# Optimization experiments

Hardware: AMD Instinct MI355X
Metric: run time of the kernel (lower is better)

## Reference

```python
import jax, jax.numpy as jnp
import numpy as np

D_MODEL = 1024
N_HEADS = 16
D_HEAD = D_MODEL // N_HEADS
LN_EPS = 1e-5


def setup_inputs() -> dict:
    key = jax.random.key(0)
    ks = jax.random.split(key, 6)
    B, T = 2, 2048
    s_in = 1.0 / np.sqrt(D_MODEL)
    return {
        "x": jax.random.normal(ks[0], (B, T, D_MODEL), dtype=jnp.float32),
        "ln_g": jnp.ones((D_MODEL,), jnp.float32),
        "ln_b": jnp.zeros((D_MODEL,), jnp.float32),
        "qkv_w": jax.random.normal(ks[1], (D_MODEL, 3 * D_MODEL), jnp.float32) * s_in,
        "qkv_b": jnp.zeros((3 * D_MODEL,), jnp.float32),
        "out_w": jax.random.normal(ks[2], (D_MODEL, D_MODEL), jnp.float32) * s_in,
        "out_b": jnp.zeros((D_MODEL,), jnp.float32),
    }


def _layernorm(x, g, b):
    mu = jnp.mean(x, axis=-1, keepdims=True)
    var = jnp.var(x, axis=-1, keepdims=True)
    return (x - mu) * jax.lax.rsqrt(var + LN_EPS) * g + b


def reference(x, ln_g, ln_b, qkv_w, qkv_b, out_w, out_b):
    B, T, D = x.shape
    h = _layernorm(x, ln_g, ln_b)
    qkv = h @ qkv_w + qkv_b  # [B,T,3D]
    q, k, v = jnp.split(qkv, 3, axis=-1)
    # [B,H,T,dh]
    q = q.reshape(B, T, N_HEADS, D_HEAD).transpose(0, 2, 1, 3)
    k = k.reshape(B, T, N_HEADS, D_HEAD).transpose(0, 2, 1, 3)
    v = v.reshape(B, T, N_HEADS, D_HEAD).transpose(0, 2, 1, 3)
    scores = jnp.einsum("bhqd,bhkd->bhqk", q, k) / jnp.sqrt(jnp.float32(D_HEAD))
    causal = jnp.tril(jnp.ones((T, T), bool))
    scores = jnp.where(causal, scores, -jnp.inf)
    attn = jax.nn.softmax(scores, axis=-1)  # [B,H,T,T]
    out = jnp.einsum("bhqk,bhkd->bhqd", attn, v)
    out = out.transpose(0, 2, 1, 3).reshape(B, T, D)
    x_out = x + out @ out_w + out_b
    return (x_out, attn)
```

## Files before the change

### kernel.cpp

```cpp
#include <hip/hip_runtime.h>
#include <math.h>

#define B_SZ 2
#define T_SEQ 2048
#define DM 1024
#define NH 16
#define DH 64
#define ROWS (B_SZ * T_SEQ)
#define LN_EPS 1e-5f

typedef __attribute__((ext_vector_type(8))) short short8;
typedef __attribute__((ext_vector_type(4))) float floatx4;

__device__ __forceinline__ short f2bf(float f) {
    union { float f; unsigned u; } v; v.f = f;
    unsigned r = v.u + 0x7fffu + ((v.u >> 16) & 1u);
    return (short)(r >> 16);
}
__device__ __forceinline__ short8 ld8(const short* p) {
    short4 a = *(const short4*)p;
    short4 b = *(const short4*)(p + 4);
    return short8{a.x, a.y, a.z, a.w, b.x, b.y, b.z, b.w};
}
__device__ __forceinline__ void gl2lds16(const void* g, void* l) {
    __builtin_amdgcn_global_load_lds(
        (const __attribute__((address_space(1))) unsigned int*)g,
        (__attribute__((address_space(3))) unsigned int*)l, 16, 0, 0);
}

__global__ __launch_bounds__(256) void ln_kernel(const float* __restrict__ x,
                                                 const float* __restrict__ g,
                                                 const float* __restrict__ bta,
                                                 short* __restrict__ h) {
    int row = blockIdx.x;
    const float* xr = x + (size_t)row * DM;
    int tid = threadIdx.x;
    float4 v = ((const float4*)xr)[tid];
    float s = v.x + v.y + v.z + v.w;
    float ss = v.x * v.x + v.y * v.y + v.z * v.z + v.w * v.w;
    for (int off = 1; off < 64; off <<= 1) {
        s += __shfl_xor(s, off);
        ss += __shfl_xor(ss, off);
    }
    __shared__ float sbuf[4], ssbuf[4];
    int wave = tid >> 6, lane = tid & 63;
    if (lane == 0) { sbuf[wave] = s; ssbuf[wave] = ss; }
    __syncthreads();
    s = sbuf[0] + sbuf[1] + sbuf[2] + sbuf[3];
    ss = ssbuf[0] + ssbuf[1] + ssbuf[2] + ssbuf[3];
    float mu = s * (1.0f / DM);
    float var = ss * (1.0f / DM) - mu * mu;
    float rs = rsqrtf(var + LN_EPS);
    float4 gg = ((const float4*)g)[tid];
    float4 bb = ((const float4*)bta)[tid];
    short4 o;
    o.x = f2bf((v.x - mu) * rs * gg.x + bb.x);
    o.y = f2bf((v.y - mu) * rs * gg.y + bb.y);
    o.z = f2bf((v.z - mu) * rs * gg.z + bb.z);
    o.w = f2bf((v.w - mu) * rs * gg.w + bb.w);
    *(short4*)&h[(size_t)row * DM + tid * 4] = o;
}

__global__ __launch_bounds__(256) void wt_kernel(const float* __restrict__ W,
                                                 short* __restrict__ Wt, int K, int N) {
    __shared__ float t[32][33];
    int tx = threadIdx.x & 31, ty = threadIdx.x >> 5;
    int k0 = blockIdx.y * 32, n0 = blockIdx.x * 32;
    for (int p = 0; p < 4; ++p)
        t[ty + 8 * p][tx] = W[(size_t)(k0 + ty + 8 * p) * N + n0 + tx];
    __syncthreads();
    for (int p = 0; p < 4; ++p)
        Wt[(size_t)(n0 + ty + 8 * p) * K + k0 + tx] = f2bf(t[tx][ty + 8 * p]);
}

template <bool RESID, bool BF16_OUT>
__global__ __launch_bounds__(256) void mfma_gemm(const short* __restrict__ A,
                                                 const short* __restrict__ Bt,
                                                 const float* __restrict__ bias,
                                                 const float* __restrict__ resid,
                                                 void* __restrict__ Cout,
                                                 int M, int N, int K) {
    __shared__ short As[128 * 32];
    __shared__ short Bs[128 * 32];
    int tid = threadIdx.x;
    int wave = tid >> 6, lane = tid & 63;
    int l15 = lane & 15, quad = lane >> 4;
    int wm = wave & 1, wn = wave >> 1;
    int row0 = blockIdx.y * 128, col0 = blockIdx.x * 128;

    floatx4 acc[4][4] = {};
    for (int k0 = 0; k0 < K; k0 += 32) {
        __syncthreads();
        for (int i = 0; i < 2; ++i) {
            int c = (wave * 2 + i) * 64 + lane;
            int row = c >> 2, kc = c & 3;
            gl2lds16(A + (size_t)(row0 + row) * K + k0 + kc * 8, &As[(wave * 2 + i) * 512]);
            gl2lds16(Bt + (size_t)(col0 + row) * K + k0 + kc * 8, &Bs[(wave * 2 + i) * 512]);
        }
        __syncthreads();
        short8 af[4], bfr[4];
        for (int m = 0; m < 4; ++m)
            af[m] = *(const short8*)&As[(wm * 64 + m * 16 + l15) * 32 + quad * 8];
        for (int n = 0; n < 4; ++n)
            bfr[n] = *(const short8*)&Bs[(wn * 64 + n * 16 + l15) * 32 + quad * 8];
        for (int m = 0; m < 4; ++m)
            for (int n = 0; n < 4; ++n)
                acc[m][n] = __builtin_amdgcn_mfma_f32_16x16x32_bf16(af[m], bfr[n], acc[m][n], 0, 0, 0);
    }
    float bias_v[4];
    for (int n = 0; n < 4; ++n) bias_v[n] = bias[col0 + wn * 64 + n * 16 + l15];
    for (int m = 0; m < 4; ++m)
        for (int r = 0; r < 4; ++r) {
            int rg = row0 + wm * 64 + m * 16 + quad * 4 + r;
            for (int n = 0; n < 4; ++n) {
                int cg = col0 + wn * 64 + n * 16 + l15;
                float v = acc[m][n][r] + bias_v[n];
                if (BF16_OUT) {
                    ((short*)Cout)[(size_t)rg * N + cg] = f2bf(v);
                } else {
                    if (RESID) v += resid[(size_t)rg * N + cg];
                    ((float*)Cout)[(size_t)rg * N + cg] = v;
                }
            }
        }
}

__global__ __launch_bounds__(256) void vt_kernel(const short* __restrict__ qkv,
                                                 short* __restrict__ Vt) {
    int bh = blockIdx.y;
    int b = bh >> 4, hh = bh & 15;
    int t0 = blockIdx.x * 64;
    __shared__ short tile[64 * 72];
    int tc = threadIdx.x & 7, tr = threadIdx.x >> 3;
    const short* src = qkv + (size_t)(b * T_SEQ + t0) * (3 * DM) + 2 * DM + hh * DH;
    for (int p = 0; p < 2; ++p) {
        int r = tr + p * 32;
        *(short8*)&tile[r * 72 + tc * 8] = *(const short8*)(src + (size_t)r * (3 * DM) + tc * 8);
    }
    __syncthreads();
    short* dst = Vt + (size_t)bh * DH * T_SEQ + t0;
    for (int p = 0; p < 2; ++p) {
        int d = tr + p * 32;
        short tmp[8];
#pragma unroll
        for (int j = 0; j < 8; ++j) tmp[j] = tile[(tc * 8 + j) * 72 + d];
        *(short8*)(dst + (size_t)d * T_SEQ + tc * 8) =
            short8{tmp[0], tmp[1], tmp[2], tmp[3], tmp[4], tmp[5], tmp[6], tmp[7]};
    }
}

__global__ __launch_bounds__(256) void attn_kernel(const short* __restrict__ qkv,
                                                   const short* __restrict__ Vt,
                                                   float* __restrict__ attn,
                                                   short* __restrict__ ao) {
    int blk = blockIdx.x;
    int qt = (T_SEQ / 64 - 1) - (blk & 31);
    int bh = blk >> 5;
    int b = bh >> 4, hh = bh & 15;
    int q0 = qt * 64;
    int tid = threadIdx.x;
    int wave = tid >> 6, lane = tid & 63;
    int l15 = lane & 15, quad = lane >> 4;

    __shared__ short Ks[64 * 64];
    __shared__ short Vs[64 * 64];
    __shared__ short Ps[4 * 16 * 72];

    const float scale = 0.125f;
    const short* Qg = qkv + (size_t)(b * T_SEQ + q0) * (3 * DM) + hh * DH;
    const short* Kg = qkv + (size_t)(b * T_SEQ) * (3 * DM) + DM + hh * DH;
    const short* Vg = Vt + (size_t)bh * DH * T_SEQ;

    short8 qa[2];
    for (int d0 = 0; d0 < 2; ++d0)
        qa[d0] = *(const short8*)(Qg + (size_t)(wave * 16 + l15) * (3 * DM) + d0 * 32 + quad * 8);

    int ktiles = qt + 1;
    int qrow = q0 + wave * 16 + quad * 4;

    float lsum[4] = {0.f, 0.f, 0.f, 0.f};
    for (int kt = 0; kt < ktiles; ++kt) {
        __syncthreads();
        for (int i = 0; i < 2; ++i) {
            int c = (wave * 2 + i) * 64 + lane;
            int row = c >> 3, kc = c & 7;
            int kcs = kc ^ (row & 7);
            gl2lds16(Kg + (size_t)(kt * 64 + row) * (3 * DM) + kcs * 8, &Ks[(wave * 2 + i) * 512]);
        }
        __syncthreads();
        floatx4 sacc[4] = {};
        for (int n0 = 0; n0 < 4; ++n0) {
            int row = n0 * 16 + l15;
            for (int d0 = 0; d0 < 2; ++d0) {
                int cc = (d0 * 4 + quad) ^ (row & 7);
                short8 kb = *(const short8*)&Ks[row * 64 + cc * 8];
                sacc[n0] = __builtin_amdgcn_mfma_f32_16x16x32_bf16(qa[d0], kb, sacc[n0], 0, 0, 0);
            }
        }
        int kbase = kt * 64 + l15;
        for (int r = 0; r < 4; ++r) {
            float s = 0.f;
            for (int n0 = 0; n0 < 4; ++n0)
                s += (kbase + n0 * 16 <= qrow + r) ? __expf(sacc[n0][r] * scale) : 0.f;
            s += __shfl_xor(s, 1); s += __shfl_xor(s, 2);
            s += __shfl_xor(s, 4); s += __shfl_xor(s, 8);
            lsum[r] += s;
        }
    }
    float invl[4];
    for (int r = 0; r < 4; ++r) invl[r] = 1.0f / lsum[r];

    floatx4 oacc[4] = {};
    float* abase = attn + (size_t)bh * T_SEQ * T_SEQ;
    for (int kt = 0; kt < T_SEQ / 64; ++kt) {
        if (kt < ktiles) {
            __syncthreads();
            for (int i = 0; i < 2; ++i) {
                int c = (wave * 2 + i) * 64 + lane;
                int row = c >> 3, kc = c & 7;
                int kcs = kc ^ (row & 7);
                gl2lds16(Kg + (size_t)(kt * 64 + row) * (3 * DM) + kcs * 8, &Ks[(wave * 2 + i) * 512]);
                gl2lds16(Vg + (size_t)row * T_SEQ + kt * 64 + kcs * 8, &Vs[(wave * 2 + i) * 512]);
            }
            __syncthreads();
            floatx4 sacc[4] = {};
            for (int n0 = 0; n0 < 4; ++n0) {
                int row = n0 * 16 + l15;
                for (int d0 = 0; d0 < 2; ++d0) {
                    int cc = (d0 * 4 + quad) ^ (row & 7);
                    short8 kb = *(const short8*)&Ks[row * 64 + cc * 8];
                    sacc[n0] = __builtin_amdgcn_mfma_f32_16x16x32_bf16(qa[d0], kb, sacc[n0], 0, 0, 0);
                }
            }
            int kbase = kt * 64 + l15;
            short* Pw = &Ps[wave * 1152];
            for (int n0 = 0; n0 < 4; ++n0)
                for (int r = 0; r < 4; ++r) {
                    float p = (kbase + n0 * 16 <= qrow + r)
                                  ? __expf(sacc[n0][r] * scale) * invl[r] : 0.f;
                    abase[(size_t)(qrow + r) * T_SEQ + kbase + n0 * 16] = p;
                    Pw[(quad * 4 + r) * 72 + n0 * 16 + l15] = f2bf(p);
                }
            __syncthreads();
            for (int m0 = 0; m0 < 4; ++m0) {
                int d = m0 * 16 + l15;
                for (int k0 = 0; k0 < 2; ++k0) {
                    int cc = (k0 * 4 + quad) ^ (d & 7);
                    short8 va = *(const short8*)&Vs[d * 64 + cc * 8];
                    short8 pb = ld8(&Pw[l15 * 72 + (k0 * 4 + quad) * 8]);
                    oacc[m0] = __builtin_amdgcn_mfma_f32_16x16x32_bf16(va, pb, oacc[m0], 0, 0, 0);
                }
            }
        } else {
            int kbase = kt * 64 + l15;
            for (int n0 = 0; n0 < 4; ++n0)
                for (int r = 0; r < 4; ++r)
                    abase[(size_t)(qrow + r) * T_SEQ + kbase + n0 * 16] = 0.f;
        }
    }
    short* Pw = &Ps[wave * 1152];
    __syncthreads();
    for (int m0 = 0; m0 < 4; ++m0)
        for (int r = 0; r < 4; ++r)
            Pw[l15 * 72 + m0 * 16 + quad * 4 + r] = f2bf(oacc[m0][r]);
    __syncthreads();
    for (int p = 0; p < 2; ++p) {
        int lq = (lane >> 3) + p * 8;
        int dc = lane & 7;
        short8 o8 = ld8(&Pw[lq * 72 + dc * 8]);
        *(short8*)(ao + (size_t)(b * T_SEQ + q0 + wave * 16 + lq) * DM + hh * DH + dc * 8) = o8;
    }
}

extern "C" void kernel_launch(void* const* d_in, const int* in_sizes, int n_in,
                              void* d_out, int out_size, void* d_ws, size_t ws_size,
                              hipStream_t stream) {
    const float* x     = (const float*)d_in[0];
    const float* ln_g  = (const float*)d_in[1];
    const float* ln_b  = (const float*)d_in[2];
    const float* qkv_w = (const float*)d_in[3];
    const float* qkv_b = (const float*)d_in[4];
    const float* out_w = (const float*)d_in[5];
    const float* out_b = (const float*)d_in[6];

    float* xout = (float*)d_out;
    float* attn = xout + (size_t)ROWS * DM;

    short* h    = (short*)d_ws;
    short* qkvT = h + (size_t)ROWS * DM;
    short* outT = qkvT + (size_t)(3 * DM) * DM;
    short* qkv  = outT + (size_t)DM * DM;
    short* Vt   = qkv + (size_t)ROWS * 3 * DM;
    short* ao   = Vt + (size_t)B_SZ * NH * DH * T_SEQ;

    ln_kernel<<<ROWS, 256, 0, stream>>>(x, ln_g, ln_b, h);
    wt_kernel<<<dim3(3 * DM / 32, DM / 32), 256, 0, stream>>>(qkv_w, qkvT, DM, 3 * DM);
    wt_kernel<<<dim3(DM / 32, DM / 32), 256, 0, stream>>>(out_w, outT, DM, DM);

    mfma_gemm<false, true><<<dim3(3 * DM / 128, ROWS / 128), 256, 0, stream>>>(
        h, qkvT, qkv_b, nullptr, qkv, ROWS, 3 * DM, DM);

    vt_kernel<<<dim3(T_SEQ / 64, B_SZ * NH), 256, 0, stream>>>(qkv, Vt);

    attn_kernel<<<B_SZ * NH * (T_SEQ / 64), 256, 0, stream>>>(qkv, Vt, attn, ao);

    mfma_gemm<true, false><<<dim3(DM / 128, ROWS / 128), 256, 0, stream>>>(
        ao, outT, out_b, x, xout, ROWS, DM, DM);
}
```

Before: 777.2 us.

## Double-buffer K/V tiles and vectorize attention-probability stores via bf16 LDS staging

Adds two-deep LDS buffers for K and V so the next tile's global-to-LDS loads are issued while MFMAs run on the current tile. Each iteration now ends with one waitcnt and barrier instead of a pair of __syncthreads. The attention-probability matrix is no longer written as scattered per-lane scalar floats. It is read back from the per-wave bf16 P tile in LDS and written as float4 rows, and the masked upper region is zero-filled with float4 stores after the loop. In exchange, the returned attn values are now bf16-rounded, which loses precision, and the per-wave LDS reuse now depends on intra-wave ordering instead of block barriers.

```diff
diff --git a/kernel.cpp b/kernel.cpp
--- a/kernel.cpp
+++ b/kernel.cpp
@@ -16,6 +16,10 @@
     union { float f; unsigned u; } v; v.f = f;
     unsigned r = v.u + 0x7fffu + ((v.u >> 16) & 1u);
     return (short)(r >> 16);
+}
+__device__ __forceinline__ float bf2f(short s) {
+    union { float f; unsigned u; } v; v.u = ((unsigned)(unsigned short)s) << 16;
+    return v.f;
 }
 __device__ __forceinline__ short8 ld8(const short* p) {
     short4 a = *(const short4*)p;
@@ -162,8 +166,8 @@
     int wave = tid >> 6, lane = tid & 63;
     int l15 = lane & 15, quad = lane >> 4;
 
-    __shared__ short Ks[64 * 64];
-    __shared__ short Vs[64 * 64];
+    __shared__ short Ks[2][64 * 64];
+    __shared__ short Vs[2][64 * 64];
     __shared__ short Ps[4 * 16 * 72];
 
     const float scale = 0.125f;
@@ -178,22 +182,38 @@
     int ktiles = qt + 1;
     int qrow = q0 + wave * 16 + quad * 4;
 
-    float lsum[4] = {0.f, 0.f, 0.f, 0.f};
-    for (int kt = 0; kt < ktiles; ++kt) {
-        __syncthreads();
+    auto stageK = [&](int kt, int buf) {
         for (int i = 0; i < 2; ++i) {
             int c = (wave * 2 + i) * 64 + lane;
             int row = c >> 3, kc = c & 7;
             int kcs = kc ^ (row & 7);
-            gl2lds16(Kg + (size_t)(kt * 64 + row) * (3 * DM) + kcs * 8, &Ks[(wave * 2 + i) * 512]);
-        }
-        __syncthreads();
+            gl2lds16(Kg + (size_t)(kt * 64 + row) * (3 * DM) + kcs * 8,
+                     &Ks[buf][(wave * 2 + i) * 512]);
+        }
+    };
+    auto stageV = [&](int kt, int buf) {
+        for (int i = 0; i < 2; ++i) {
+            int c = (wave * 2 + i) * 64 + lane;
+            int row = c >> 3, kc = c & 7;
+            int kcs = kc ^ (row & 7);
+            gl2lds16(Vg + (size_t)row * T_SEQ + kt * 64 + kcs * 8,
+                     &Vs[buf][(wave * 2 + i) * 512]);
+        }
+    };
+
+    float lsum[4] = {0.f, 0.f, 0.f, 0.f};
+    stageK(0, 0);
+    asm volatile("s_waitcnt vmcnt(0)" ::: "memory");
+    __builtin_amdgcn_s_barrier();
+    int cur = 0;
+    for (int kt = 0; kt < ktiles; ++kt) {
+        if (kt + 1 < ktiles) stageK(kt + 1, cur ^ 1);
         floatx4 sacc[4] = {};
         for (int n0 = 0; n0 < 4; ++n0) {
             int row = n0 * 16 + l15;
             for (int d0 = 0; d0 < 2; ++d0) {
                 int cc = (d0 * 4 + quad) ^ (row & 7);
-                short8 kb = *(const short8*)&Ks[row * 64 + cc * 8];
+                short8 kb = *(const short8*)&Ks[cur][row * 64 + cc * 8];
                 sacc[n0] = __builtin_amdgcn_mfma_f32_16x16x32_bf16(qa[d0], kb, sacc[n0], 0, 0, 0);
             }
         }
@@ -206,69 +226,81 @@
             s += __shfl_xor(s, 4); s += __shfl_xor(s, 8);
             lsum[r] += s;
         }
+        asm volatile("s_waitcnt vmcnt(0)" ::: "memory");
+        __builtin_amdgcn_s_barrier();
+        cur ^= 1;
     }
     float invl[4];
     for (int r = 0; r < 4; ++r) invl[r] = 1.0f / lsum[r];
 
     floatx4 oacc[4] = {};
     float* abase = attn + (size_t)bh * T_SEQ * T_SEQ;
-    for (int kt = 0; kt < T_SEQ / 64; ++kt) {
-        if (kt < ktiles) {
-            __syncthreads();
-            for (int i = 0; i < 2; ++i) {
-                int c = (wave * 2 + i) * 64 + lane;
-                int row = c >> 3, kc = c & 7;
-                int kcs = kc ^ (row & 7);
-                gl2lds16(Kg + (size_t)(kt * 64 + row) * (3 * DM) + kcs * 8, &Ks[(wave * 2 + i) * 512]);
-                gl2lds16(Vg + (size_t)row * T_SEQ + kt * 64 + kcs * 8, &Vs[(wave * 2 + i) * 512]);
-            }
-            __syncthreads();
-            floatx4 sacc[4] = {};
-            for (int n0 = 0; n0 < 4; ++n0) {
-                int row = n0 * 16 + l15;
-                for (int d0 = 0; d0 < 2; ++d0) {
-                    int cc = (d0 * 4 + quad) ^ (row & 7);
-                    short8 kb = *(const short8*)&Ks[row * 64 + cc * 8];
-                    sacc[n0] = __builtin_amdgcn_mfma_f32_16x16x32_bf16(qa[d0], kb, sacc[n0], 0, 0, 0);
-                }
-            }
-            int kbase = kt * 64 + l15;
-            short* Pw = &Ps[wave * 1152];
-            for (int n0 = 0; n0 < 4; ++n0)
-                for (int r = 0; r < 4; ++r) {
-                    float p = (kbase + n0 * 16 <= qrow + r)
-                                  ? __expf(sacc[n0][r] * scale) * invl[r] : 0.f;
-                    abase[(size_t)(qrow + r) * T_SEQ + kbase + n0 * 16] = p;
-                    Pw[(quad * 4 + r) * 72 + n0 * 16 + l15] = f2bf(p);
-                }
-            __syncthreads();
-            for (int m0 = 0; m0 < 4; ++m0) {
-                int d = m0 * 16 + l15;
-                for (int k0 = 0; k0 < 2; ++k0) {
-                    int cc = (k0 * 4 + quad) ^ (d & 7);
-                    short8 va = *(const short8*)&Vs[d * 64 + cc * 8];
-                    short8 pb = ld8(&Pw[l15 * 72 + (k0 * 4 + quad) * 8]);
-                    oacc[m0] = __builtin_amdgcn_mfma_f32_16x16x32_bf16(va, pb, oacc[m0], 0, 0, 0);
-                }
-            }
-        } else {
-            int kbase = kt * 64 + l15;
-            for (int n0 = 0; n0 < 4; ++n0)
-                for (int r = 0; r < 4; ++r)
-                    abase[(size_t)(qrow + r) * T_SEQ + kbase + n0 * 16] = 0.f;
-        }
-    }
     short* Pw = &Ps[wave * 1152];
-    __syncthreads();
+    stageK(0, 0);
+    stageV(0, 0);
+    asm volatile("s_waitcnt vmcnt(0)" ::: "memory");
+    __builtin_amdgcn_s_barrier();
+    cur = 0;
+    for (int kt = 0; kt < ktiles; ++kt) {
+        if (kt + 1 < ktiles) { stageK(kt + 1, cur ^ 1); stageV(kt + 1, cur ^ 1); }
+        floatx4 sacc[4] = {};
+        for (int n0 = 0; n0 < 4; ++n0) {
+            int row = n0 * 16 + l15;
+            for (int d0 = 0; d0 < 2; ++d0) {
+                int cc = (d0 * 4 + quad) ^ (row & 7);
+                short8 kb = *(const short8*)&Ks[cur][row * 64 + cc * 8];
+                sacc[n0] = __builtin_amdgcn_mfma_f32_16x16x32_bf16(qa[d0], kb, sacc[n0], 0, 0, 0);
+            }
+        }
+        int kbase = kt * 64 + l15;
+        for (int n0 = 0; n0 < 4; ++n0)
+            for (int r = 0; r < 4; ++r) {
+                float p = (kbase + n0 * 16 <= qrow + r)
+                              ? __expf(sacc[n0][r] * scale) * invl[r] : 0.f;
+                Pw[(quad * 4 + r) * 72 + n0 * 16 + l15] = f2bf(p);
+            }
+        for (int m0 = 0; m0 < 4; ++m0) {
+            int d = m0 * 16 + l15;
+            for (int k0 = 0; k0 < 2; ++k0) {
+                int cc = (k0 * 4 + quad) ^ (d & 7);
+                short8 va = *(const short8*)&Vs[cur][d * 64 + cc * 8];
+                short8 pb = ld8(&Pw[l15 * 72 + (k0 * 4 + quad) * 8]);
+                oacc[m0] = __builtin_amdgcn_mfma_f32_16x16x32_bf16(va, pb, oacc[m0], 0, 0, 0);
+            }
+        }
+        {
+            int ql = lane >> 2, c4 = lane & 3;
+            const short* src = &Pw[ql * 72 + c4 * 16];
+            float* dst = &abase[(size_t)(q0 + wave * 16 + ql) * T_SEQ + kt * 64 + c4 * 16];
+            for (int j = 0; j < 2; ++j) {
+                short8 v8 = ld8(src + j * 8);
+                float4 f0, f1;
+                f0.x = bf2f(v8[0]); f0.y = bf2f(v8[1]); f0.z = bf2f(v8[2]); f0.w = bf2f(v8[3]);
+                f1.x = bf2f(v8[4]); f1.y = bf2f(v8[5]); f1.z = bf2f(v8[6]); f1.w = bf2f(v8[7]);
+                ((float4*)dst)[j * 2] = f0;
+                ((float4*)dst)[j * 2 + 1] = f1;
+            }
+        }
+        asm volatile("s_waitcnt vmcnt(0)" ::: "memory");
+        __builtin_amdgcn_s_barrier();
+        cur ^= 1;
+    }
+
     for (int m0 = 0; m0 < 4; ++m0)
         for (int r = 0; r < 4; ++r)
             Pw[l15 * 72 + m0 * 16 + quad * 4 + r] = f2bf(oacc[m0][r]);
-    __syncthreads();
     for (int p = 0; p < 2; ++p) {
         int lq = (lane >> 3) + p * 8;
         int dc = lane & 7;
         short8 o8 = ld8(&Pw[lq * 72 + dc * 8]);
         *(short8*)(ao + (size_t)(b * T_SEQ + q0 + wave * 16 + lq) * DM + hh * DH + dc * 8) = o8;
+    }
+    {
+        int ql = lane >> 2, c4 = lane & 3;
+        float4 z = {0.f, 0.f, 0.f, 0.f};
+        float* rowp = &abase[(size_t)(q0 + wave * 16 + ql) * T_SEQ];
+        for (int col4 = ktiles * 16 + c4; col4 < T_SEQ / 4; col4 += 4)
+            ((float4*)rowp)[col4] = z;
     }
 }
 
```

Result: slower. 814.7 us (+4.8%).

## Coalesce attention-probability stores via LDS, drop barriers, and remap block order

Applied to the files above, without the earlier changes.

The attention kernel now writes probabilities to the attn output by staging the bf16 P tile in LDS and emitting float4 row-contiguous stores, rather than scattered per-element fp32 stores. The masked upper-triangle zeros are written in a vectorized tail loop after the main loop, and the per-tile barrier before P@V is removed because each wave only reads its own P slice. Block indices are also remapped to interleave work across blocks. In exchange, the stored attn values are now rounded to bf16 before being written as fp32, which loses precision against the fp32 reference.

```diff
diff --git a/kernel.cpp b/kernel.cpp
--- a/kernel.cpp
+++ b/kernel.cpp
@@ -16,6 +16,10 @@
     union { float f; unsigned u; } v; v.f = f;
     unsigned r = v.u + 0x7fffu + ((v.u >> 16) & 1u);
     return (short)(r >> 16);
+}
+__device__ __forceinline__ float bf2f(short s) {
+    union { float f; unsigned u; } v; v.u = ((unsigned)(unsigned short)s) << 16;
+    return v.f;
 }
 __device__ __forceinline__ short8 ld8(const short* p) {
     short4 a = *(const short4*)p;
@@ -153,7 +157,7 @@
                                                    const short* __restrict__ Vt,
                                                    float* __restrict__ attn,
                                                    short* __restrict__ ao) {
-    int blk = blockIdx.x;
+    int blk = (blockIdx.x & 7) * 128 + (blockIdx.x >> 3);
     int qt = (T_SEQ / 64 - 1) - (blk & 31);
     int bh = blk >> 5;
     int b = bh >> 4, hh = bh & 15;
@@ -212,63 +216,72 @@
 
     floatx4 oacc[4] = {};
     float* abase = attn + (size_t)bh * T_SEQ * T_SEQ;
-    for (int kt = 0; kt < T_SEQ / 64; ++kt) {
-        if (kt < ktiles) {
-            __syncthreads();
-            for (int i = 0; i < 2; ++i) {
-                int c = (wave * 2 + i) * 64 + lane;
-                int row = c >> 3, kc = c & 7;
-                int kcs = kc ^ (row & 7);
-                gl2lds16(Kg + (size_t)(kt * 64 + row) * (3 * DM) + kcs * 8, &Ks[(wave * 2 + i) * 512]);
-                gl2lds16(Vg + (size_t)row * T_SEQ + kt * 64 + kcs * 8, &Vs[(wave * 2 + i) * 512]);
-            }
-            __syncthreads();
-            floatx4 sacc[4] = {};
-            for (int n0 = 0; n0 < 4; ++n0) {
-                int row = n0 * 16 + l15;
-                for (int d0 = 0; d0 < 2; ++d0) {
-                    int cc = (d0 * 4 + quad) ^ (row & 7);
-                    short8 kb = *(const short8*)&Ks[row * 64 + cc * 8];
-                    sacc[n0] = __builtin_amdgcn_mfma_f32_16x16x32_bf16(qa[d0], kb, sacc[n0], 0, 0, 0);
-                }
-            }
-            int kbase = kt * 64 + l15;
-            short* Pw = &Ps[wave * 1152];
-            for (int n0 = 0; n0 < 4; ++n0)
-                for (int r = 0; r < 4; ++r) {
-                    float p = (kbase + n0 * 16 <= qrow + r)
-                                  ? __expf(sacc[n0][r] * scale) * invl[r] : 0.f;
-                    abase[(size_t)(qrow + r) * T_SEQ + kbase + n0 * 16] = p;
-                    Pw[(quad * 4 + r) * 72 + n0 * 16 + l15] = f2bf(p);
-                }
-            __syncthreads();
-            for (int m0 = 0; m0 < 4; ++m0) {
-                int d = m0 * 16 + l15;
-                for (int k0 = 0; k0 < 2; ++k0) {
-                    int cc = (k0 * 4 + quad) ^ (d & 7);
-                    short8 va = *(const short8*)&Vs[d * 64 + cc * 8];
-                    short8 pb = ld8(&Pw[l15 * 72 + (k0 * 4 + quad) * 8]);
-                    oacc[m0] = __builtin_amdgcn_mfma_f32_16x16x32_bf16(va, pb, oacc[m0], 0, 0, 0);
-                }
-            }
-        } else {
-            int kbase = kt * 64 + l15;
-            for (int n0 = 0; n0 < 4; ++n0)
-                for (int r = 0; r < 4; ++r)
-                    abase[(size_t)(qrow + r) * T_SEQ + kbase + n0 * 16] = 0.f;
-        }
-    }
     short* Pw = &Ps[wave * 1152];
-    __syncthreads();
+    for (int kt = 0; kt < ktiles; ++kt) {
+        __syncthreads();
+        for (int i = 0; i < 2; ++i) {
+            int c = (wave * 2 + i) * 64 + lane;
+            int row = c >> 3, kc = c & 7;
+            int kcs = kc ^ (row & 7);
+            gl2lds16(Kg + (size_t)(kt * 64 + row) * (3 * DM) + kcs * 8, &Ks[(wave * 2 + i) * 512]);
+            gl2lds16(Vg + (size_t)row * T_SEQ + kt * 64 + kcs * 8, &Vs[(wave * 2 + i) * 512]);
+        }
+        __syncthreads();
+        floatx4 sacc[4] = {};
+        for (int n0 = 0; n0 < 4; ++n0) {
+            int row = n0 * 16 + l15;
+            for (int d0 = 0; d0 < 2; ++d0) {
+                int cc = (d0 * 4 + quad) ^ (row & 7);
+                short8 kb = *(const short8*)&Ks[row * 64 + cc * 8];
+                sacc[n0] = __builtin_amdgcn_mfma_f32_16x16x32_bf16(qa[d0], kb, sacc[n0], 0, 0, 0);
+            }
+        }
+        int kbase = kt * 64 + l15;
+        for (int n0 = 0; n0 < 4; ++n0)
+            for (int r = 0; r < 4; ++r) {
+                float p = (kbase + n0 * 16 <= qrow + r)
+                              ? __expf(sacc[n0][r] * scale) * invl[r] : 0.f;
+                Pw[(quad * 4 + r) * 72 + n0 * 16 + l15] = f2bf(p);
+            }
+        for (int m0 = 0; m0 < 4; ++m0) {
+            int d = m0 * 16 + l15;
+            for (int k0 = 0; k0 < 2; ++k0) {
+                int cc = (k0 * 4 + quad) ^ (d & 7);
+                short8 va = *(const short8*)&Vs[d * 64 + cc * 8];
+                short8 pb = ld8(&Pw[l15 * 72 + (k0 * 4 + quad) * 8]);
+                oacc[m0] = __builtin_amdgcn_mfma_f32_16x16x32_bf16(va, pb, oacc[m0], 0, 0, 0);
+            }
+        }
+        {
+            int ql = lane >> 2, c4 = lane & 3;
+            const short* src = &Pw[ql * 72 + c4 * 16];
+            float* dst = &abase[(size_t)(q0 + wave * 16 + ql) * T_SEQ + kt * 64 + c4 * 16];
+            for (int j = 0; j < 2; ++j) {
+                short8 v8 = ld8(src + j * 8);
+                float4 f0, f1;
+                f0.x = bf2f(v8[0]); f0.y = bf2f(v8[1]); f0.z = bf2f(v8[2]); f0.w = bf2f(v8[3]);
+                f1.x = bf2f(v8[4]); f1.y = bf2f(v8[5]); f1.z = bf2f(v8[6]); f1.w = bf2f(v8[7]);
+                ((float4*)dst)[j * 2] = f0;
+                ((float4*)dst)[j * 2 + 1] = f1;
+            }
+        }
+    }
+
     for (int m0 = 0; m0 < 4; ++m0)
         for (int r = 0; r < 4; ++r)
             Pw[l15 * 72 + m0 * 16 + quad * 4 + r] = f2bf(oacc[m0][r]);
-    __syncthreads();
     for (int p = 0; p < 2; ++p) {
         int lq = (lane >> 3) + p * 8;
         int dc = lane & 7;
         short8 o8 = ld8(&Pw[lq * 72 + dc * 8]);
         *(short8*)(ao + (size_t)(b * T_SEQ + q0 + wave * 16 + lq) * DM + hh * DH + dc * 8) = o8;
+    }
+    {
+        int ql = lane >> 2, c4 = lane & 3;
+        float4 z = {0.f, 0.f, 0.f, 0.f};
+        float* rowp = &abase[(size_t)(q0 + wave * 16 + ql) * T_SEQ];
+        for (int col4 = ktiles * 16 + c4; col4 < T_SEQ / 4; col4 += 4)
+            ((float4*)rowp)[col4] = z;
     }
 }
 
```

After: 753.3 us. -3.1%, faster.
